# Kernel optimization log

Hardware: AMD Instinct MI355X
Metric: run time of the kernel (lower is better)

Reference implementation:

```python
import jax, jax.numpy as jnp
import numpy as np

B, C, N, K, OUT = 8, 128, 8192, 16, 128

def setup_inputs() -> dict:
    key = jax.random.key(0)
    k1, k2, k3, k4 = jax.random.split(key, 4)
    x = jax.random.normal(k1, (B, C, N), dtype=jnp.float32)
    idx = jax.random.randint(k2, (B * N * K,), 0, B * N, dtype=jnp.int64)
    W = jax.random.normal(k3, (OUT, C, 1), dtype=jnp.float32) * 0.05
    b = jax.random.normal(k4, (OUT,), dtype=jnp.float32) * 0.05
    return {"x": x, "idx": idx, "W": W, "b": b}

def reference(x, idx, W, b):
    Bs, Cs, Ns = x.shape
    k = idx.shape[0] // (Bs * Ns)
    # (B,C,N) -> (B*N, C) matching torch permute(0,2,1).reshape(-1,C)
    x_flat = jnp.transpose(x, (0, 2, 1)).reshape(-1, Cs)
    # gather k neighbors per point, then max over neighbor dim
    neighbors = x_flat[idx].reshape(Bs, Ns, k, Cs)  # (B,N,k,C)
    agg = neighbors.max(axis=2)                      # (B,N,C)
    # 1x1 conv == per-point linear: (B,N,C) x (O,C) -> (B,O,N)
    out = jnp.einsum('bnc,oc->bon', agg, W[:, :, 0]) + b[None, :, None]
    return jax.nn.relu(out)
```

## Files before the change

### kernel.cpp

```cpp
#include <hip/hip_runtime.h>
#include <stdint.h>

#define B_  8
#define C_  128
#define N_  8192
#define K_  16
#define O_  128
#define TP  32

typedef __attribute__((ext_vector_type(8))) short short8;
typedef __attribute__((ext_vector_type(4))) float f32x4;

__device__ __forceinline__ unsigned short f2bf(float f) {
    union { float f; uint32_t u; } v; v.f = f;
    uint32_t u = v.u;
    return (unsigned short)((u + 0x7FFFu + ((u >> 16) & 1u)) >> 16);
}
__device__ __forceinline__ uint32_t fwdmap(uint32_t u) {
    uint32_t s  = u & 0x80008000u;
    uint32_t xm = s - (s >> 15) + 0x80008000u;
    return u ^ xm;
}
__device__ __forceinline__ uint32_t invmap(uint32_t v) {
    uint32_t s  = (~v) & 0x80008000u;
    uint32_t xm = s - (s >> 15) + 0x80008000u;
    return v ^ xm;
}
__device__ __forceinline__ uint32_t pkmax(uint32_t a, uint32_t b) {
    uint32_t d;
    asm("v_pk_max_u16 %0, %1, %2" : "=v"(d) : "v"(a), "v"(b));
    return d;
}
__device__ __forceinline__ uint4 pkmax4(uint4 a, uint4 b) {
    return make_uint4(pkmax(a.x, b.x), pkmax(a.y, b.y),
                      pkmax(a.z, b.z), pkmax(a.w, b.w));
}

template<bool PREW>
__global__ __launch_bounds__(256) void k_transpose(const float* __restrict__ x,
                                                   unsigned short* __restrict__ xt,
                                                   const float* __restrict__ Wp,
                                                   unsigned short* __restrict__ Wbf) {
    int blk = blockIdx.x;
    if (PREW && blk == 1024) {
        int t = threadIdx.x;
        #pragma unroll
        for (int i = 0; i < 32; ++i) {
            int e = t + i * 256;
            float2 w2 = ((const float2*)Wp)[e];
            ((uint32_t*)Wbf)[e] = (uint32_t)f2bf(w2.x) | ((uint32_t)f2bf(w2.y) << 16);
        }
        return;
    }
    __shared__ uint32_t lds[64 * 66];
    int t    = threadIdx.x;
    int lane = t & 63;
    int wv   = t >> 6;
    int b    = blk >> 7;
    int n0   = (blk & 127) * 64;

    const float* xb = x + (size_t)b * C_ * N_ + n0 + lane;
    #pragma unroll
    for (int j = 0; j < 16; ++j) {
        int c2 = wv * 16 + j;
        float f0 = xb[(size_t)(2 * c2) * N_];
        float f1 = xb[(size_t)(2 * c2 + 1) * N_];
        uint32_t pk = (uint32_t)f2bf(f0) | ((uint32_t)f2bf(f1) << 16);
        lds[c2 * 66 + lane] = fwdmap(pk);
    }
    __syncthreads();

    int rl = lane >> 4;
    int ch = lane & 15;
    #pragma unroll
    for (int it = 0; it < 4; ++it) {
        int r = it * 16 + wv * 4 + rl;
        uint32_t u0 = lds[(ch * 4 + 0) * 66 + r];
        uint32_t u1 = lds[(ch * 4 + 1) * 66 + r];
        uint32_t u2 = lds[(ch * 4 + 2) * 66 + r];
        uint32_t u3 = lds[(ch * 4 + 3) * 66 + r];
        *(uint4*)(xt + ((size_t)(b * N_ + n0 + r)) * C_ + ch * 8) =
            make_uint4(u0, u1, u2, u3);
    }
}

template<bool PREW>
__global__ __launch_bounds__(256, 4) void k_main(const unsigned short* __restrict__ xt,
                                                 const int* __restrict__ idx,
                                                 const float* __restrict__ Wp,
                                                 const unsigned short* __restrict__ Wbf,
                                                 const float* __restrict__ bp,
                                                 float* __restrict__ out) {
    __shared__ __align__(16) unsigned short agg[TP * 136];
    __shared__ int idxs[TP * K_];

    int t    = threadIdx.x;
    int lane = t & 63;
    int wv   = t >> 6;
    int blk  = blockIdx.x;
    int b    = blk >> 8;
    int n0   = (blk & 255) * TP;
    size_t pbase = (size_t)b * N_ + n0;

    const int* ip = idx + pbase * K_;
    idxs[t]       = __builtin_nontemporal_load(ip + t);
    idxs[t + 256] = __builtin_nontemporal_load(ip + t + 256);
    __syncthreads();

    int pt  = lane >> 4;
    int cch = lane & 15;
    #pragma unroll
    for (int i = 0; i < 2; ++i) {
        int p = wv * 8 + i * 4 + pt;
        const int* qq = &idxs[p * K_];
        uint4 d[16];
        #pragma unroll
        for (int k = 0; k < 16; ++k)
            d[k] = *(const uint4*)(xt + (size_t)qq[k] * C_ + cch * 8);
        #pragma unroll
        for (int s = 8; s >= 1; s >>= 1)
            #pragma unroll
            for (int k = 0; k < s; ++k)
                d[k] = pkmax4(d[k], d[k + s]);
        uint4 v = make_uint4(invmap(d[0].x), invmap(d[0].y),
                             invmap(d[0].z), invmap(d[0].w));
        *(uint4*)&agg[p * 136 + cch * 8] = v;
    }
    __syncthreads();

    int r16 = lane & 15;
    int h   = lane >> 4;
    int wo  = wv * 32;
    const size_t ob = (size_t)b * O_ * N_ + n0;

    #pragma unroll
    for (int ot2 = 0; ot2 < 2; ++ot2) {
        short8 af[4];
        if (PREW) {
            #pragma unroll
            for (int kk = 0; kk < 4; ++kk)
                af[kk] = *(const short8*)(Wbf + (size_t)(wo + ot2 * 16 + r16) * C_ + kk * 32 + h * 8);
        } else {
            #pragma unroll
            for (int kk = 0; kk < 4; ++kk) {
                const float* wr = Wp + (size_t)(wo + ot2 * 16 + r16) * C_ + kk * 32 + h * 8;
                float4 a0 = *(const float4*)wr;
                float4 a1 = *(const float4*)(wr + 4);
                short8 s;
                s[0] = (short)f2bf(a0.x); s[1] = (short)f2bf(a0.y);
                s[2] = (short)f2bf(a0.z); s[3] = (short)f2bf(a0.w);
                s[4] = (short)f2bf(a1.x); s[5] = (short)f2bf(a1.y);
                s[6] = (short)f2bf(a1.z); s[7] = (short)f2bf(a1.w);
                af[kk] = s;
            }
        }
        float4 bv = *(const float4*)(bp + wo + ot2 * 16 + h * 4);
        int orow = wo + ot2 * 16 + h * 4;
        #pragma unroll
        for (int pt2 = 0; pt2 < 2; ++pt2) {
            short8 bfr[4];
            #pragma unroll
            for (int kk = 0; kk < 4; ++kk)
                bfr[kk] = *(const short8*)&agg[(pt2 * 16 + r16) * 136 + kk * 32 + h * 8];
            f32x4 acc = {0.f, 0.f, 0.f, 0.f};
            #pragma unroll
            for (int kk = 0; kk < 4; ++kk)
                acc = __builtin_amdgcn_mfma_f32_16x16x32_bf16(af[kk], bfr[kk], acc, 0, 0, 0);
            float* op = out + ob + (size_t)orow * N_ + pt2 * 16 + r16;
            __builtin_nontemporal_store(fmaxf(acc[0] + bv.x, 0.f), op);
            __builtin_nontemporal_store(fmaxf(acc[1] + bv.y, 0.f), op + (size_t)N_);
            __builtin_nontemporal_store(fmaxf(acc[2] + bv.z, 0.f), op + (size_t)2 * N_);
            __builtin_nontemporal_store(fmaxf(acc[3] + bv.w, 0.f), op + (size_t)3 * N_);
        }
    }
}

extern "C" void kernel_launch(void* const* d_in, const int* in_sizes, int n_in,
                              void* d_out, int out_size, void* d_ws, size_t ws_size,
                              hipStream_t stream) {
    (void)in_sizes; (void)n_in; (void)out_size;
    const float* x    = (const float*)d_in[0];
    const int*   idx  = (const int*)d_in[1];
    const float* W    = (const float*)d_in[2];
    const float* bias = (const float*)d_in[3];
    float* out = (float*)d_out;

    const size_t XTB = (size_t)B_ * N_ * C_ * 2;
    unsigned short* xt  = (unsigned short*)d_ws;
    unsigned short* wbf = (unsigned short*)((char*)d_ws + XTB);
    bool prew = ws_size >= XTB + O_ * C_ * 2;

    if (prew) {
        hipLaunchKernelGGL(k_transpose<true>,  dim3(1025), dim3(256), 0, stream, x, xt, W, wbf);
        hipLaunchKernelGGL(k_main<true>,       dim3(2048), dim3(256), 0, stream, xt, idx, W, wbf, bias, out);
    } else {
        hipLaunchKernelGGL(k_transpose<false>, dim3(1024), dim3(256), 0, stream, x, xt, W, wbf);
        hipLaunchKernelGGL(k_main<false>,      dim3(2048), dim3(256), 0, stream, xt, idx, W, wbf, bias, out);
    }
}
```

Baseline: 50.14 us.

## Split features into channel planes and gather per plane with XCD-affine blocks

The transposed bf16 features are stored as four 32-channel planes of 4 MB each. A separate gather kernel assigns each XCD to a single plane, so the random neighbour reads stay inside a working set that can fit in that XCD's L2. The max-aggregated result is written to a plane-split buffer, and a third kernel runs the MFMA GEMM with bias and ReLU from it. This adds an extra kernel launch and a round trip of the aggregated tensor through global memory, and it relies on blocks being dispatched round-robin across the 8 XCDs. It also needs twice the workspace, otherwise the code falls back to the old two-kernel fused path.

```diff
diff --git a/kernel.cpp b/kernel.cpp
--- a/kernel.cpp
+++ b/kernel.cpp
@@ -1,15 +1,18 @@
 #include <hip/hip_runtime.h>
 #include <stdint.h>
 
-#define B_  8
-#define C_  128
-#define N_  8192
-#define K_  16
-#define O_  128
-#define TP  32
+#define B_   8
+#define C_   128
+#define N_   8192
+#define K_   16
+#define O_   128
+#define NP   65536
+#define PL32 ((size_t)NP * 32)
+#define TPF  32
 
 typedef __attribute__((ext_vector_type(8))) short short8;
 typedef __attribute__((ext_vector_type(4))) float f32x4;
+typedef __attribute__((ext_vector_type(4))) uint32_t u32x4;
 
 __device__ __forceinline__ unsigned short f2bf(float f) {
     union { float f; uint32_t u; } v; v.f = f;
@@ -36,13 +39,13 @@
                       pkmax(a.z, b.z), pkmax(a.w, b.w));
 }
 
-template<bool PREW>
-__global__ __launch_bounds__(256) void k_transpose(const float* __restrict__ x,
-                                                   unsigned short* __restrict__ xt,
-                                                   const float* __restrict__ Wp,
-                                                   unsigned short* __restrict__ Wbf) {
+
+__global__ __launch_bounds__(256) void k_transpose_pl(const float* __restrict__ x,
+                                                      unsigned short* __restrict__ xt,
+                                                      const float* __restrict__ Wp,
+                                                      unsigned short* __restrict__ Wbf) {
     int blk = blockIdx.x;
-    if (PREW && blk == 1024) {
+    if (blk == 1024) {
         int t = threadIdx.x;
         #pragma unroll
         for (int i = 0; i < 32; ++i) {
@@ -70,6 +73,148 @@
     }
     __syncthreads();
 
+    int rr = lane >> 2;
+    int ch = lane & 3;
+    size_t rowb = (size_t)(b * N_ + n0);
+    #pragma unroll
+    for (int pl = 0; pl < 4; ++pl) {
+        int r = wv * 16 + rr;
+        uint32_t u0 = lds[(pl * 16 + ch * 4 + 0) * 66 + r];
+        uint32_t u1 = lds[(pl * 16 + ch * 4 + 1) * 66 + r];
+        uint32_t u2 = lds[(pl * 16 + ch * 4 + 2) * 66 + r];
+        uint32_t u3 = lds[(pl * 16 + ch * 4 + 3) * 66 + r];
+        *(uint4*)(xt + (size_t)pl * PL32 + (rowb + r) * 32 + ch * 8) =
+            make_uint4(u0, u1, u2, u3);
+    }
+}
+
+__global__ __launch_bounds__(256, 4) void k_gather(const unsigned short* __restrict__ xt,
+                                                   const int* __restrict__ idx,
+                                                   unsigned short* __restrict__ agg4) {
+    __shared__ int idxs[K_ * 128];
+    int t    = threadIdx.x;
+    int lane = t & 63;
+    int wv   = t >> 6;
+    int blk  = blockIdx.x;
+    int xcd  = blk & 7;
+    int g    = xcd & 3;
+    int h    = xcd >> 2;
+    int tile = blk >> 3;
+    int p0   = h * 32768 + tile * 128;
+
+    const int* ip = idx + (size_t)p0 * K_;
+    #pragma unroll
+    for (int i = 0; i < 8; ++i) {
+        int e = t + i * 256;
+        int pl_ = e & 127, k = e >> 7;
+        idxs[k * 128 + pl_] = __builtin_nontemporal_load(ip + pl_ * K_ + k);
+    }
+    __syncthreads();
+
+    const unsigned short* plane  = xt   + (size_t)g * PL32;
+    unsigned short*       aplane = agg4 + (size_t)g * PL32;
+    int pt = lane >> 2;
+    int c4 = lane & 3;
+    #pragma unroll
+    for (int pass = 0; pass < 2; ++pass) {
+        int pl_ = wv * 32 + pass * 16 + pt;
+        const unsigned short* basep = plane + c4 * 8;
+        uint4 d[16];
+        #pragma unroll
+        for (int k = 0; k < 16; ++k) {
+            int q = idxs[k * 128 + pl_];
+            d[k] = *(const uint4*)(basep + (size_t)q * 32);
+        }
+        #pragma unroll
+        for (int s = 8; s >= 1; s >>= 1)
+            #pragma unroll
+            for (int k = 0; k < s; ++k)
+                d[k] = pkmax4(d[k], d[k + s]);
+        u32x4 v;
+        v[0] = invmap(d[0].x); v[1] = invmap(d[0].y);
+        v[2] = invmap(d[0].z); v[3] = invmap(d[0].w);
+        __builtin_nontemporal_store(v, (u32x4*)(aplane + (size_t)(p0 + pl_) * 32 + c4 * 8));
+    }
+}
+
+__global__ __launch_bounds__(256) void k_gemm(const unsigned short* __restrict__ agg4,
+                                              const unsigned short* __restrict__ Wbf,
+                                              const float* __restrict__ bp,
+                                              float* __restrict__ out) {
+    int t    = threadIdx.x;
+    int lane = t & 63;
+    int wv   = t >> 6;
+    int blk  = blockIdx.x;
+    int p0   = blk * 64;
+    int b    = p0 >> 13;
+    int n0   = p0 & (N_ - 1);
+    int r16  = lane & 15;
+    int h    = lane >> 4;
+    int wo   = wv * 32;
+    const size_t ob = (size_t)b * O_ * N_ + n0;
+
+    #pragma unroll
+    for (int ot2 = 0; ot2 < 2; ++ot2) {
+        short8 af[4];
+        #pragma unroll
+        for (int kk = 0; kk < 4; ++kk)
+            af[kk] = *(const short8*)(Wbf + (size_t)(wo + ot2 * 16 + r16) * C_ + kk * 32 + h * 8);
+        float4 bv = *(const float4*)(bp + wo + ot2 * 16 + h * 4);
+        int orow = wo + ot2 * 16 + h * 4;
+        #pragma unroll
+        for (int pt2 = 0; pt2 < 4; ++pt2) {
+            short8 bfr[4];
+            #pragma unroll
+            for (int kk = 0; kk < 4; ++kk)
+                bfr[kk] = *(const short8*)(agg4 + (size_t)kk * PL32
+                                           + (size_t)(p0 + pt2 * 16 + r16) * 32 + h * 8);
+            f32x4 acc = {0.f, 0.f, 0.f, 0.f};
+            #pragma unroll
+            for (int kk = 0; kk < 4; ++kk)
+                acc = __builtin_amdgcn_mfma_f32_16x16x32_bf16(af[kk], bfr[kk], acc, 0, 0, 0);
+            float* op = out + ob + (size_t)orow * N_ + pt2 * 16 + r16;
+            __builtin_nontemporal_store(fmaxf(acc[0] + bv.x, 0.f), op);
+            __builtin_nontemporal_store(fmaxf(acc[1] + bv.y, 0.f), op + (size_t)N_);
+            __builtin_nontemporal_store(fmaxf(acc[2] + bv.z, 0.f), op + (size_t)2 * N_);
+            __builtin_nontemporal_store(fmaxf(acc[3] + bv.w, 0.f), op + (size_t)3 * N_);
+        }
+    }
+}
+
+
+template<bool PREW>
+__global__ __launch_bounds__(256) void k_transpose_flat(const float* __restrict__ x,
+                                                        unsigned short* __restrict__ xt,
+                                                        const float* __restrict__ Wp,
+                                                        unsigned short* __restrict__ Wbf) {
+    int blk = blockIdx.x;
+    if (PREW && blk == 1024) {
+        int t = threadIdx.x;
+        #pragma unroll
+        for (int i = 0; i < 32; ++i) {
+            int e = t + i * 256;
+            float2 w2 = ((const float2*)Wp)[e];
+            ((uint32_t*)Wbf)[e] = (uint32_t)f2bf(w2.x) | ((uint32_t)f2bf(w2.y) << 16);
+        }
+        return;
+    }
+    __shared__ uint32_t lds[64 * 66];
+    int t    = threadIdx.x;
+    int lane = t & 63;
+    int wv   = t >> 6;
+    int b    = blk >> 7;
+    int n0   = (blk & 127) * 64;
+
+    const float* xb = x + (size_t)b * C_ * N_ + n0 + lane;
+    #pragma unroll
+    for (int j = 0; j < 16; ++j) {
+        int c2 = wv * 16 + j;
+        float f0 = xb[(size_t)(2 * c2) * N_];
+        float f1 = xb[(size_t)(2 * c2 + 1) * N_];
+        uint32_t pk = (uint32_t)f2bf(f0) | ((uint32_t)f2bf(f1) << 16);
+        lds[c2 * 66 + lane] = fwdmap(pk);
+    }
+    __syncthreads();
     int rl = lane >> 4;
     int ch = lane & 15;
     #pragma unroll
@@ -85,21 +230,21 @@
 }
 
 template<bool PREW>
-__global__ __launch_bounds__(256, 4) void k_main(const unsigned short* __restrict__ xt,
-                                                 const int* __restrict__ idx,
-                                                 const float* __restrict__ Wp,
-                                                 const unsigned short* __restrict__ Wbf,
-                                                 const float* __restrict__ bp,
-                                                 float* __restrict__ out) {
-    __shared__ __align__(16) unsigned short agg[TP * 136];
-    __shared__ int idxs[TP * K_];
+__global__ __launch_bounds__(256, 4) void k_fused(const unsigned short* __restrict__ xt,
+                                                  const int* __restrict__ idx,
+                                                  const float* __restrict__ Wp,
+                                                  const unsigned short* __restrict__ Wbf,
+                                                  const float* __restrict__ bp,
+                                                  float* __restrict__ out) {
+    __shared__ __align__(16) unsigned short agg[TPF * 136];
+    __shared__ int idxs[TPF * K_];
 
     int t    = threadIdx.x;
     int lane = t & 63;
     int wv   = t >> 6;
     int blk  = blockIdx.x;
     int b    = blk >> 8;
-    int n0   = (blk & 255) * TP;
+    int n0   = (blk & 255) * TPF;
     size_t pbase = (size_t)b * N_ + n0;
 
     const int* ip = idx + pbase * K_;
@@ -185,16 +330,24 @@
     const float* bias = (const float*)d_in[3];
     float* out = (float*)d_out;
 
-    const size_t XTB = (size_t)B_ * N_ * C_ * 2;
-    unsigned short* xt  = (unsigned short*)d_ws;
-    unsigned short* wbf = (unsigned short*)((char*)d_ws + XTB);
-    bool prew = ws_size >= XTB + O_ * C_ * 2;
-
-    if (prew) {
-        hipLaunchKernelGGL(k_transpose<true>,  dim3(1025), dim3(256), 0, stream, x, xt, W, wbf);
-        hipLaunchKernelGGL(k_main<true>,       dim3(2048), dim3(256), 0, stream, xt, idx, W, wbf, bias, out);
+    const size_t PLB = (size_t)4 * PL32 * 2;
+    const size_t WB  = (size_t)O_ * C_ * 2;
+
+    if (ws_size >= 2 * PLB + WB) {
+        unsigned short* xt   = (unsigned short*)d_ws;
+        unsigned short* agg4 = (unsigned short*)((char*)d_ws + PLB);
+        unsigned short* wbf  = (unsigned short*)((char*)d_ws + 2 * PLB);
+        hipLaunchKernelGGL(k_transpose_pl, dim3(1025), dim3(256), 0, stream, x, xt, W, wbf);
+        hipLaunchKernelGGL(k_gather,       dim3(2048), dim3(256), 0, stream, xt, idx, agg4);
+        hipLaunchKernelGGL(k_gemm,         dim3(1024), dim3(256), 0, stream, agg4, wbf, bias, out);
+    } else if (ws_size >= PLB + WB) {
+        unsigned short* xt  = (unsigned short*)d_ws;
+        unsigned short* wbf = (unsigned short*)((char*)d_ws + PLB);
+        hipLaunchKernelGGL(k_transpose_flat<true>, dim3(1025), dim3(256), 0, stream, x, xt, W, wbf);
+        hipLaunchKernelGGL(k_fused<true>,          dim3(2048), dim3(256), 0, stream, xt, idx, W, wbf, bias, out);
     } else {
-        hipLaunchKernelGGL(k_transpose<false>, dim3(1024), dim3(256), 0, stream, x, xt, W, wbf);
-        hipLaunchKernelGGL(k_main<false>,      dim3(2048), dim3(256), 0, stream, xt, idx, W, wbf, bias, out);
-    }
-}
+        unsigned short* xt = (unsigned short*)d_ws;
+        hipLaunchKernelGGL(k_transpose_flat<false>, dim3(1024), dim3(256), 0, stream, x, xt, W, nullptr);
+        hipLaunchKernelGGL(k_fused<false>,          dim3(2048), dim3(256), 0, stream, xt, idx, W, nullptr, bias, out);
+    }
+}
```

Measured after the change: 79.38 us. +58.3%, slower.
